# Optimization experiments

Hardware: AMD Instinct MI355X
Metric: run time of the kernel (lower is better)

## Reference

```python
import jax, jax.numpy as jnp
import numpy as np

LAT_SIZE = 2048
BATCH = 4096


def cos_pos_encoding_1d(size, freq_div=2.0, sub_freq_max=4.0):
    freqs = list(range(1, int(size / freq_div)))
    spaces = [np.linspace(0, freq * 2 * np.pi, size) for freq in freqs]
    sub_freqs = [1.0 / float(i) for i in range(2, int(sub_freq_max))]
    sub_spaces = [np.linspace(i * freq * 2 * np.pi, (i + 1) * freq * 2 * np.pi, size)
                  for freq in sub_freqs for i in range(int(1 / freq))]
    spaces = spaces + sub_spaces
    cos = [np.cos(space) for space in spaces]
    return np.stack(cos).astype(np.float32)  # (n_freq, size)


def setup_inputs() -> dict:
    key = jax.random.key(0)
    k1, k2 = jax.random.split(key)
    cos_basis = jnp.asarray(cos_pos_encoding_1d(LAT_SIZE, 1, 8))  # (2074, 2048)
    n_freq = cos_basis.shape[0]
    x = jax.random.normal(k1, (BATCH, LAT_SIZE), dtype=jnp.float32)
    # nn.Linear default init: U(-1/sqrt(in), 1/sqrt(in))
    bound = 1.0 / np.sqrt(LAT_SIZE)
    W = jax.random.uniform(k2, (n_freq, LAT_SIZE), dtype=jnp.float32,
                           minval=-bound, maxval=bound)
    return {"x": x, "W": W, "cos_basis": cos_basis}


def reference(x, W, cos_basis):
    # x: (B, lat), W: (n_freq, lat), cos_basis: (n_freq, lat)
    x_freqs = x @ W.T                          # (B, n_freq)  -- to_freq_size
    # broadcast-mul + sum over freq dim == GEMM against fixed cosine basis
    out = x_freqs @ cos_basis                  # (B, lat)
    # global max-normalize (norm=True)
    return out / jnp.max(out)
```

## Files before the change

kernel.cpp:

```cpp
#include <hip/hip_runtime.h>
#include <hip/hip_bf16.h>
#include <cstdint>

#define BATCH 4096
#define LAT   2048
#define NFREQ 2074
#define KPAD  2112

typedef __bf16 bf16x8 __attribute__((ext_vector_type(8)));
typedef float  f32x4  __attribute__((ext_vector_type(4)));

__device__ __forceinline__ unsigned short f2bf(float f) {
    unsigned int u = __float_as_uint(f);
    u = (u + 0x7fffu + ((u >> 16) & 1u)) >> 16;
    return (unsigned short)u;
}

__device__ __forceinline__ void gload_lds16(const unsigned short* g, unsigned short* l) {
    __builtin_amdgcn_global_load_lds(
        (const __attribute__((address_space(1))) unsigned int*)g,
        (__attribute__((address_space(3))) unsigned int*)l,
        16, 0, 0);
}

__global__ void prep_kernel(const float* __restrict__ x,
                            const float* __restrict__ W,
                            const float* __restrict__ cb,
                            unsigned short* __restrict__ xb,
                            unsigned short* __restrict__ WT,
                            unsigned short* __restrict__ cosT,
                            float* __restrict__ maxp) {
    __shared__ float t[64][65];
    const int bid = blockIdx.x;
    const int tid = threadIdx.x;
    if (bid < 4096) {
        int i = bid * 256 + tid;
        const float4* x4 = (const float4*)x;
        float4 a = x4[2 * i];
        float4 b = x4[2 * i + 1];
        union { unsigned short us[8]; uint4 v; } p;
        p.us[0] = f2bf(a.x); p.us[1] = f2bf(a.y); p.us[2] = f2bf(a.z); p.us[3] = f2bf(a.w);
        p.us[4] = f2bf(b.x); p.us[5] = f2bf(b.y); p.us[6] = f2bf(b.z); p.us[7] = f2bf(b.w);
        ((uint4*)xb)[i] = p.v;
        if (i == 0) *maxp = -__builtin_inff();
        return;
    }
    int b2 = bid - 4096;
    const float* in     = (b2 < 1056) ? W  : cb;
    unsigned short* out = (b2 < 1056) ? WT : cosT;
    if (b2 >= 1056) b2 -= 1056;
    const int c0 = (b2 % 32) * 64;
    const int r0 = (b2 / 32) * 64;
    for (int i = tid; i < 4096; i += 256) {
        int rr = i >> 6, cc = i & 63;
        int r = r0 + rr;
        float v = (r < NFREQ) ? in[(size_t)r * LAT + c0 + cc] : 0.0f;
        t[rr][cc] = v;
    }
    __syncthreads();
    for (int i = tid; i < 4096; i += 256) {
        int cc = i >> 6, rr = i & 63;
        out[(size_t)(c0 + cc) * KPAD + (r0 + rr)] = f2bf(t[rr][cc]);
    }
}

template <int N, int K>
__global__ __launch_bounds__(256, 2)
void gemm1_kernel(const unsigned short* __restrict__ A,
                  const unsigned short* __restrict__ Bt,
                  unsigned short* __restrict__ C) {
    __shared__ alignas(16) unsigned short As[3][128 * 32];
    __shared__ alignas(16) unsigned short Bs[3][64 * 32];

    const int tid  = threadIdx.x;
    const int wave = tid >> 6;
    const int lane = tid & 63;
    const int wm   = (wave >> 1) * 64;
    const int wn   = (wave & 1) * 32;
    const int quad = lane >> 4;
    const int l16  = lane & 15;

    const int mBase = blockIdx.y * 128;
    const int nBase = blockIdx.x * 64;

    const int srow = lane >> 2;
    const int sk   = (lane & 3) * 8;

    const unsigned short* Ab1 = A  + (size_t)(mBase + (wave * 2 + 0) * 16 + srow) * K + sk;
    const unsigned short* Ab2 = A  + (size_t)(mBase + (wave * 2 + 1) * 16 + srow) * K + sk;
    const unsigned short* Bb1 = Bt + (size_t)(nBase + wave * 16 + srow) * K + sk;

    const int aoff1 = ((wave * 2 + 0) * 16) * 32;
    const int aoff2 = ((wave * 2 + 1) * 16) * 32;
    const int boff  = (wave * 16) * 32;

    constexpr int NIT = K / 32;
    gload_lds16(Ab1, &As[0][aoff1]);
    gload_lds16(Ab2, &As[0][aoff2]);
    gload_lds16(Bb1, &Bs[0][boff]);

    f32x4 acc[4][2] = {};
    int bc = 0;
    for (int j = 0; j < NIT; ++j) {
        const int bn = (bc == 2) ? 0 : bc + 1;
        if (j + 1 < NIT) {
            const int k0 = (j + 1) * 32;
            gload_lds16(Ab1 + k0, &As[bn][aoff1]);
            gload_lds16(Ab2 + k0, &As[bn][aoff2]);
            gload_lds16(Bb1 + k0, &Bs[bn][boff]);
            asm volatile("s_waitcnt vmcnt(3)\n\ts_barrier" ::: "memory");
        } else {
            asm volatile("s_waitcnt vmcnt(0)\n\ts_barrier" ::: "memory");
        }
        bf16x8 af[4], bfr[2];
#pragma unroll
        for (int mi = 0; mi < 4; ++mi)
            af[mi] = *(const bf16x8*)&As[bc][(wm + mi * 16 + l16) * 32 + quad * 8];
#pragma unroll
        for (int ni = 0; ni < 2; ++ni)
            bfr[ni] = *(const bf16x8*)&Bs[bc][(wn + ni * 16 + l16) * 32 + quad * 8];
#pragma unroll
        for (int mi = 0; mi < 4; ++mi)
#pragma unroll
            for (int ni = 0; ni < 2; ++ni)
                acc[mi][ni] = __builtin_amdgcn_mfma_f32_16x16x32_bf16(
                    af[mi], bfr[ni], acc[mi][ni], 0, 0, 0);
        bc = bn;
    }

#pragma unroll
    for (int mi = 0; mi < 4; ++mi)
#pragma unroll
        for (int ni = 0; ni < 2; ++ni) {
            int col = nBase + wn + ni * 16 + l16;
#pragma unroll
            for (int r = 0; r < 4; ++r) {
                int row = mBase + wm + mi * 16 + quad * 4 + r;
                C[(size_t)row * N + col] = f2bf(acc[mi][ni][r]);
            }
        }
}

template <int N, int K>
__global__ __launch_bounds__(512, 4)
void gemm2_kernel(const unsigned short* __restrict__ A,
                  const unsigned short* __restrict__ Bt,
                  float* __restrict__ C,
                  float* __restrict__ maxp) {
    __shared__ alignas(16) unsigned short As[3][128 * 32];
    __shared__ alignas(16) unsigned short Bs[3][128 * 32];
    __shared__ float redbuf[8];

    const int tid  = threadIdx.x;
    const int wave = tid >> 6;
    const int lane = tid & 63;
    const int wm   = (wave >> 2) * 64;
    const int wn   = (wave & 3) * 32;
    const int quad = lane >> 4;
    const int l16  = lane & 15;

    const int mBase = blockIdx.y * 128;
    const int nBase = blockIdx.x * 128;

    const int srow = lane >> 2;
    const int sk   = (lane & 3) * 8;

    const unsigned short* Ab1 = A  + (size_t)(mBase + wave * 16 + srow) * K + sk;
    const unsigned short* Bb1 = Bt + (size_t)(nBase + wave * 16 + srow) * K + sk;
    const int coff = (wave * 16) * 32;

    constexpr int NIT = K / 32;
    gload_lds16(Ab1, &As[0][coff]);
    gload_lds16(Bb1, &Bs[0][coff]);

    f32x4 acc[4][2] = {};
    int bc = 0;
    for (int j = 0; j < NIT; ++j) {
        const int bn = (bc == 2) ? 0 : bc + 1;
        if (j + 1 < NIT) {
            const int k0 = (j + 1) * 32;
            gload_lds16(Ab1 + k0, &As[bn][coff]);
            gload_lds16(Bb1 + k0, &Bs[bn][coff]);
            asm volatile("s_waitcnt vmcnt(2)\n\ts_barrier" ::: "memory");
        } else {
            asm volatile("s_waitcnt vmcnt(0)\n\ts_barrier" ::: "memory");
        }
        bf16x8 af[4], bfr[2];
#pragma unroll
        for (int mi = 0; mi < 4; ++mi)
            af[mi] = *(const bf16x8*)&As[bc][(wm + mi * 16 + l16) * 32 + quad * 8];
#pragma unroll
        for (int ni = 0; ni < 2; ++ni)
            bfr[ni] = *(const bf16x8*)&Bs[bc][(wn + ni * 16 + l16) * 32 + quad * 8];
#pragma unroll
        for (int mi = 0; mi < 4; ++mi)
#pragma unroll
            for (int ni = 0; ni < 2; ++ni)
                acc[mi][ni] = __builtin_amdgcn_mfma_f32_16x16x32_bf16(
                    af[mi], bfr[ni], acc[mi][ni], 0, 0, 0);
        bc = bn;
    }

    float vmax = -__builtin_inff();
#pragma unroll
    for (int mi = 0; mi < 4; ++mi)
#pragma unroll
        for (int ni = 0; ni < 2; ++ni) {
            int col = nBase + wn + ni * 16 + l16;
#pragma unroll
            for (int r = 0; r < 4; ++r) {
                int row = mBase + wm + mi * 16 + quad * 4 + r;
                float v = acc[mi][ni][r];
                C[(size_t)row * N + col] = v;
                vmax = fmaxf(vmax, v);
            }
        }
#pragma unroll
    for (int off = 32; off > 0; off >>= 1)
        vmax = fmaxf(vmax, __shfl_xor(vmax, off));
    if (lane == 0) redbuf[wave] = vmax;
    __syncthreads();
    if (tid == 0) {
        float m = redbuf[0];
#pragma unroll
        for (int w = 1; w < 8; ++w) m = fmaxf(m, redbuf[w]);
        if (m >= 0.0f) atomicMax((int*)maxp, __float_as_int(m));
        else           atomicMin((unsigned int*)maxp, __float_as_uint(m));
    }
}

__global__ void scale_kernel(float* __restrict__ out, const float* __restrict__ maxp) {
    int i = blockIdx.x * blockDim.x + threadIdx.x;
    float inv = 1.0f / (*maxp);
    float4* o4 = (float4*)out;
    float4 v = o4[i];
    v.x *= inv; v.y *= inv; v.z *= inv; v.w *= inv;
    o4[i] = v;
}

extern "C" void kernel_launch(void* const* d_in, const int* in_sizes, int n_in,
                              void* d_out, int out_size, void* d_ws, size_t ws_size,
                              hipStream_t stream) {
    const float* x  = (const float*)d_in[0];
    const float* W  = (const float*)d_in[1];
    const float* cb = (const float*)d_in[2];

    char* ws = (char*)d_ws;
    unsigned short* xb   = (unsigned short*)ws;
    unsigned short* WT   = (unsigned short*)(ws + (size_t)BATCH * LAT * 2);
    unsigned short* cosT = (unsigned short*)((char*)WT + (size_t)LAT * KPAD * 2);
    unsigned short* C1   = (unsigned short*)((char*)cosT + (size_t)LAT * KPAD * 2);
    float*          maxp = (float*)((char*)C1 + (size_t)LAT * LAT * 2);
    float*          out  = (float*)d_out;

    prep_kernel<<<4096 + 2 * 1056, 256, 0, stream>>>(x, W, cb, xb, WT, cosT, maxp);

    gemm1_kernel<LAT, KPAD>
        <<<dim3(LAT / 64, LAT / 128), 256, 0, stream>>>(cosT, WT, C1);

    gemm2_kernel<LAT, LAT>
        <<<dim3(LAT / 128, BATCH / 128), 512, 0, stream>>>(xb, C1, out, maxp);

    scale_kernel<<<(out_size / 4) / 256, 256, 0, stream>>>(out, maxp);
}
```

Baseline: 203.2 us.

## Split-K the basis-product GEMM into three partial slices plus a combine kernel

The first GEMM (cos basis times W, 2048x2048 over K=2112) now uses 128x128 tiles with 512 threads, split along K into three slices of 22 iterations each. Each slice writes fp32 partials, and a new combine kernel sums them and converts to bf16. The larger tile cuts redundant operand loads, and split-K restores the block count lost to the bigger tiles (768 blocks), so the GPU stays busy. In exchange it writes and reads roughly 48 MB of fp32 partials and adds an extra kernel launch.

```diff
diff --git a/kernel.cpp b/kernel.cpp
--- a/kernel.cpp
+++ b/kernel.cpp
@@ -64,40 +64,36 @@
     }
 }
 
-template <int N, int K>
-__global__ __launch_bounds__(256, 2)
-void gemm1_kernel(const unsigned short* __restrict__ A,
-                  const unsigned short* __restrict__ Bt,
-                  unsigned short* __restrict__ C) {
+template <int N, int K, int NIT>
+__global__ __launch_bounds__(512, 6)
+void gemm1_splitk_kernel(const unsigned short* __restrict__ A,
+                         const unsigned short* __restrict__ Bt,
+                         float* __restrict__ Cp) {
     __shared__ alignas(16) unsigned short As[3][128 * 32];
-    __shared__ alignas(16) unsigned short Bs[3][64 * 32];
+    __shared__ alignas(16) unsigned short Bs[3][128 * 32];
 
     const int tid  = threadIdx.x;
     const int wave = tid >> 6;
     const int lane = tid & 63;
-    const int wm   = (wave >> 1) * 64;
-    const int wn   = (wave & 1) * 32;
+    const int wm   = (wave >> 2) * 64;
+    const int wn   = (wave & 3) * 32;
     const int quad = lane >> 4;
     const int l16  = lane & 15;
 
     const int mBase = blockIdx.y * 128;
-    const int nBase = blockIdx.x * 64;
+    const int nBase = blockIdx.x * 128;
+    const int kOff  = blockIdx.z * (NIT * 32);
+    float* C = Cp + (size_t)blockIdx.z * N * N;
 
     const int srow = lane >> 2;
     const int sk   = (lane & 3) * 8;
 
-    const unsigned short* Ab1 = A  + (size_t)(mBase + (wave * 2 + 0) * 16 + srow) * K + sk;
-    const unsigned short* Ab2 = A  + (size_t)(mBase + (wave * 2 + 1) * 16 + srow) * K + sk;
-    const unsigned short* Bb1 = Bt + (size_t)(nBase + wave * 16 + srow) * K + sk;
-
-    const int aoff1 = ((wave * 2 + 0) * 16) * 32;
-    const int aoff2 = ((wave * 2 + 1) * 16) * 32;
-    const int boff  = (wave * 16) * 32;
-
-    constexpr int NIT = K / 32;
-    gload_lds16(Ab1, &As[0][aoff1]);
-    gload_lds16(Ab2, &As[0][aoff2]);
-    gload_lds16(Bb1, &Bs[0][boff]);
+    const unsigned short* Ab = A  + (size_t)(mBase + wave * 16 + srow) * K + kOff + sk;
+    const unsigned short* Bb = Bt + (size_t)(nBase + wave * 16 + srow) * K + kOff + sk;
+    const int coff = (wave * 16) * 32;
+
+    gload_lds16(Ab, &As[0][coff]);
+    gload_lds16(Bb, &Bs[0][coff]);
 
     f32x4 acc[4][2] = {};
     int bc = 0;
@@ -105,10 +101,9 @@
         const int bn = (bc == 2) ? 0 : bc + 1;
         if (j + 1 < NIT) {
             const int k0 = (j + 1) * 32;
-            gload_lds16(Ab1 + k0, &As[bn][aoff1]);
-            gload_lds16(Ab2 + k0, &As[bn][aoff2]);
-            gload_lds16(Bb1 + k0, &Bs[bn][boff]);
-            asm volatile("s_waitcnt vmcnt(3)\n\ts_barrier" ::: "memory");
+            gload_lds16(Ab + k0, &As[bn][coff]);
+            gload_lds16(Bb + k0, &Bs[bn][coff]);
+            asm volatile("s_waitcnt vmcnt(2)\n\ts_barrier" ::: "memory");
         } else {
             asm volatile("s_waitcnt vmcnt(0)\n\ts_barrier" ::: "memory");
         }
@@ -136,9 +131,29 @@
 #pragma unroll
             for (int r = 0; r < 4; ++r) {
                 int row = mBase + wm + mi * 16 + quad * 4 + r;
-                C[(size_t)row * N + col] = f2bf(acc[mi][ni][r]);
+                C[(size_t)row * N + col] = acc[mi][ni][r];
             }
         }
+}
+
+__global__ void combine_kernel(const float* __restrict__ p0,
+                               const float* __restrict__ p1,
+                               const float* __restrict__ p2,
+                               unsigned short* __restrict__ out) {
+    int i = blockIdx.x * blockDim.x + threadIdx.x;
+    const float4* a4 = (const float4*)p0;
+    const float4* b4 = (const float4*)p1;
+    const float4* c4 = (const float4*)p2;
+    union { unsigned short us[8]; uint4 v; } p;
+#pragma unroll
+    for (int h = 0; h < 2; ++h) {
+        float4 a = a4[2 * i + h], b = b4[2 * i + h], c = c4[2 * i + h];
+        p.us[4 * h + 0] = f2bf(a.x + b.x + c.x);
+        p.us[4 * h + 1] = f2bf(a.y + b.y + c.y);
+        p.us[4 * h + 2] = f2bf(a.z + b.z + c.z);
+        p.us[4 * h + 3] = f2bf(a.w + b.w + c.w);
+    }
+    ((uint4*)out)[i] = p.v;
 }
 
 template <int N, int K>
@@ -250,13 +265,17 @@
     unsigned short* WT   = (unsigned short*)(ws + (size_t)BATCH * LAT * 2);
     unsigned short* cosT = (unsigned short*)((char*)WT + (size_t)LAT * KPAD * 2);
     unsigned short* C1   = (unsigned short*)((char*)cosT + (size_t)LAT * KPAD * 2);
-    float*          maxp = (float*)((char*)C1 + (size_t)LAT * LAT * 2);
+    float*          C1p  = (float*)((char*)C1 + (size_t)LAT * LAT * 2);
+    float*          maxp = (float*)((char*)C1p + 3 * (size_t)LAT * LAT * 4);
     float*          out  = (float*)d_out;
 
     prep_kernel<<<4096 + 2 * 1056, 256, 0, stream>>>(x, W, cb, xb, WT, cosT, maxp);
 
-    gemm1_kernel<LAT, KPAD>
-        <<<dim3(LAT / 64, LAT / 128), 256, 0, stream>>>(cosT, WT, C1);
+    gemm1_splitk_kernel<LAT, KPAD, 22>
+        <<<dim3(LAT / 128, LAT / 128, 3), 512, 0, stream>>>(cosT, WT, C1p);
+
+    combine_kernel<<<(LAT * LAT / 8) / 256, 256, 0, stream>>>(
+        C1p, C1p + (size_t)LAT * LAT, C1p + 2 * (size_t)LAT * LAT, C1);
 
     gemm2_kernel<LAT, LAT>
         <<<dim3(LAT / 128, BATCH / 128), 512, 0, stream>>>(xb, C1, out, maxp);
```

Result: no change. 203.5 us (+0.1%).
